# Optimization experiments

Hardware: AMD Instinct MI355X
Metric: run time of the kernel (lower is better)

The kernel has to match this reference:

```python
import jax, jax.numpy as jnp
import numpy as np

D_MODEL = 512
HIDDEN = 2048
N_EXPERTS = 8
TOP_K = 2


def setup_inputs() -> dict:
    key = jax.random.key(0)
    ks = jax.random.split(key, 7)
    B, S = 4, 2048
    s1 = 1.0 / np.sqrt(D_MODEL)
    s2 = 1.0 / np.sqrt(HIDDEN)
    return {
        "x": jax.random.normal(ks[0], (B, S, D_MODEL), dtype=jnp.float32),
        "W1": jax.random.normal(ks[1], (N_EXPERTS, D_MODEL, HIDDEN), dtype=jnp.float32) * s1,
        "b1": jnp.zeros((N_EXPERTS, HIDDEN), dtype=jnp.float32),
        "W2": jax.random.normal(ks[2], (N_EXPERTS, HIDDEN, D_MODEL), dtype=jnp.float32) * s2,
        "b2": jnp.zeros((N_EXPERTS, D_MODEL), dtype=jnp.float32),
        "Wg": jax.random.normal(ks[3], (D_MODEL, N_EXPERTS), dtype=jnp.float32) * s1,
        "bg": jnp.zeros((N_EXPERTS,), dtype=jnp.float32),
    }


def reference(x, W1, b1, W2, b2, Wg, bg):
    # Gate: [B,S,E]
    gate_scores = jnp.einsum("bsd,de->bse", x, Wg) + bg
    topk_scores, topk_idx = jax.lax.top_k(gate_scores, TOP_K)   # [B,S,K]
    topk_weights = jax.nn.softmax(topk_scores, axis=-1)          # [B,S,K]

    # Naive MoE: compute every expert on every token (dropout is identity in eval).
    h = jax.nn.relu(jnp.einsum("bsd,edh->bseh", x, W1) + b1)     # [B,S,E,H]
    expert_outputs = jnp.einsum("bseh,ehd->bsed", h, W2) + b2    # [B,S,E,D]

    # Gather top-k expert outputs and combine.
    topk_out = jnp.take_along_axis(expert_outputs, topk_idx[..., None], axis=-2)  # [B,S,K,D]
    return jnp.sum(topk_out * topk_weights[..., None], axis=-2)  # [B,S,D]
```

## Files before the change

kernel.cpp:

```cpp
#include <hip/hip_runtime.h>
#include <hip/hip_bf16.h>
#include <cstdint>
#include <cstddef>

#define D_MODEL 512
#define HIDDEN  2048
#define N_EXP   8
#define NTOK    8192
#define MAXROWS (NTOK * 2)

typedef unsigned short u16;
typedef _Float16 half8 __attribute__((ext_vector_type(8)));
typedef float   f32x16 __attribute__((ext_vector_type(16)));

__device__ __forceinline__ unsigned pk2(_Float16 a, _Float16 b) {
    unsigned short ua, ub;
    __builtin_memcpy(&ua, &a, 2); __builtin_memcpy(&ub, &b, 2);
    return (unsigned)ua | ((unsigned)ub << 16);
}
__device__ __forceinline__ void split2(float a, float b, unsigned& h, unsigned& l) {
    _Float16 ha = (_Float16)a, hb = (_Float16)b;
    float ra = a - (float)ha, rb = b - (float)hb;
    h = pk2(ha, hb);
    l = pk2((_Float16)ra, (_Float16)rb);
}
__device__ __forceinline__ half8 h8(uint2 lo, uint2 hi) {
    union { unsigned u[4]; half8 h; } t;
    t.u[0] = lo.x; t.u[1] = lo.y; t.u[2] = hi.x; t.u[3] = hi.y;
    return t.h;
}
__device__ __forceinline__ f32x16 mfma16(half8 a, half8 b, f32x16 c) {
    return __builtin_amdgcn_mfma_f32_32x32x16_f16(a, b, c, 0, 0, 0);
}
__device__ __forceinline__ void gload16(const void* g, void* l) {
    __builtin_amdgcn_global_load_lds(
        (const __attribute__((address_space(1))) unsigned int*)g,
        (__attribute__((address_space(3))) unsigned int*)l, 16, 0, 0);
}

__global__ __launch_bounds__(256) void gate_kernel(
    const float* __restrict__ x, const float* __restrict__ Wg,
    const float* __restrict__ bg,
    int* __restrict__ eidx, float* __restrict__ ewt, int* __restrict__ cnt)
{
    const int wid  = threadIdx.x >> 6;
    const int lane = threadIdx.x & 63;
    const int t = blockIdx.x * 4 + wid;
    const float* xr = x + (size_t)t * D_MODEL;

    float p[8] = {0.f,0.f,0.f,0.f,0.f,0.f,0.f,0.f};
    for (int i = lane; i < D_MODEL; i += 64) {
        const float xv = xr[i];
        const float4 a = *(const float4*)(Wg + (size_t)i * 8);
        const float4 b = *(const float4*)(Wg + (size_t)i * 8 + 4);
        p[0] += xv*a.x; p[1] += xv*a.y; p[2] += xv*a.z; p[3] += xv*a.w;
        p[4] += xv*b.x; p[5] += xv*b.y; p[6] += xv*b.z; p[7] += xv*b.w;
    }
    #pragma unroll
    for (int off = 32; off >= 1; off >>= 1) {
        #pragma unroll
        for (int e = 0; e < 8; ++e) p[e] += __shfl_xor(p[e], off, 64);
    }
    if (lane == 0) {
        float s[8];
        #pragma unroll
        for (int e = 0; e < 8; ++e) s[e] = p[e] + bg[e];
        int e1 = 0; float v1 = s[0];
        #pragma unroll
        for (int e = 1; e < 8; ++e) if (s[e] > v1) { v1 = s[e]; e1 = e; }
        int e2 = -1; float v2 = -3.0e38f;
        #pragma unroll
        for (int e = 0; e < 8; ++e) if (e != e1 && s[e] > v2) { v2 = s[e]; e2 = e; }
        const float w1 = 1.f / (1.f + expf(v2 - v1));
        eidx[2*t]   = e1;  eidx[2*t+1] = e2;
        ewt [2*t]   = w1;  ewt [2*t+1] = 1.f - w1;
        atomicAdd(&cnt[e1], 1);
        atomicAdd(&cnt[e2], 1);
    }
}

__global__ void scan_kernel(const int* __restrict__ cnt,
                            int* __restrict__ offs, int* __restrict__ cur)
{
    if (threadIdx.x == 0) {
        int run = 0;
        #pragma unroll
        for (int e = 0; e < 8; ++e) { offs[e] = run; cur[e] = run; run += cnt[e]; }
    }
}

__global__ __launch_bounds__(256) void route_kernel(
    const int* __restrict__ eidx, const float* __restrict__ ewt,
    int* __restrict__ cur, int* __restrict__ rows, float* __restrict__ rwt)
{
    const int t = blockIdx.x * 256 + threadIdx.x;
    if (t >= NTOK) return;
    #pragma unroll
    for (int k = 0; k < 2; ++k) {
        const int e = eidx[2*t + k];
        const int pos = atomicAdd(&cur[e], 1);
        rows[pos] = t;
        rwt [pos] = ewt[2*t + k];
    }
}

__global__ __launch_bounds__(256) void conv_w1(const float* __restrict__ W1,
                                               u16* __restrict__ W1c)
{
    const int e = blockIdx.z;
    const int h0 = blockIdx.x * 64, d0 = blockIdx.y * 64;
    __shared__ float T[64][65];
    const int hl = threadIdx.x & 63, q = threadIdx.x >> 6;
    const float* src = W1 + (size_t)e * D_MODEL * HIDDEN;
    #pragma unroll
    for (int rr = 0; rr < 16; ++rr) {
        const int d = rr*4 + q;
        T[d][hl] = src[(size_t)(d0 + d) * HIDDEN + h0 + hl];
    }
    __syncthreads();
    #pragma unroll
    for (int it = 0; it < 2; ++it) {
        const int dblk = q + 4*it;
        float v[8];
        #pragma unroll
        for (int j = 0; j < 8; ++j) v[j] = T[dblk*8 + j][hl];
        unsigned hh[4], ll[4];
        #pragma unroll
        for (int p = 0; p < 4; ++p) split2(v[2*p], v[2*p+1], hh[p], ll[p]);
        const int gd = d0 + dblk*8, gh = h0 + hl;
        const int hc = gh >> 9, hloc = gh & 511;
        const int ds = gd >> 7, pa = (gd >> 4) & 7, dcb = (gd >> 3) & 1;
        u16* dst = W1c + ((size_t)(((e*4 + hc)*4 + ds)*8 + pa))*16384
                       + dcb*4096 + hloc*8;
        *(uint4*)dst          = make_uint4(hh[0], hh[1], hh[2], hh[3]);
        *(uint4*)(dst + 8192) = make_uint4(ll[0], ll[1], ll[2], ll[3]);
    }
}

__global__ __launch_bounds__(256) void conv_w2(const float* __restrict__ W2,
                                               u16* __restrict__ W2c)
{
    const int e = blockIdx.z;
    const int h0 = blockIdx.x * 64, d0 = blockIdx.y * 64;
    __shared__ float T[64][65];
    const int c63 = threadIdx.x & 63, q = threadIdx.x >> 6;
    const float* src = W2 + (size_t)e * HIDDEN * D_MODEL;
    #pragma unroll
    for (int rr = 0; rr < 16; ++rr) {
        const int h = rr*4 + q;
        T[h][c63] = src[(size_t)(h0 + h) * D_MODEL + d0 + c63];
    }
    __syncthreads();
    #pragma unroll
    for (int it = 0; it < 2; ++it) {
        const int cc = it*256 + threadIdx.x;
        const int hbl = cc >> 5, dp = cc & 31;
        unsigned hh[4], ll[4];
        #pragma unroll
        for (int dd = 0; dd < 2; ++dd) {
            split2(T[hbl*4+0][dp*2+dd], T[hbl*4+1][dp*2+dd], hh[dd*2+0], ll[dd*2+0]);
            split2(T[hbl*4+2][dp*2+dd], T[hbl*4+3][dp*2+dd], hh[dd*2+1], ll[dd*2+1]);
        }
        const int gh = h0 + hbl*4, gd = d0 + dp*2;
        const int hc = gh >> 9, pb = (gh >> 4) & 31, hb = (gh >> 2) & 3;
        u16* dst = W2c + ((size_t)((e*4 + hc)*32 + pb))*16384 + hb*2048 + gd*4;
        *(uint4*)dst          = make_uint4(hh[0], hh[1], hh[2], hh[3]);
        *(uint4*)(dst + 8192) = make_uint4(ll[0], ll[1], ll[2], ll[3]);
    }
}

__global__ __launch_bounds__(512, 2) void moe_mfma(
    const float* __restrict__ x,
    const u16* __restrict__ W1c, const u16* __restrict__ W2c,
    const float* __restrict__ b1, const float* __restrict__ b2,
    const int* __restrict__ cnt, const int* __restrict__ offs,
    const int* __restrict__ rows, const float* __restrict__ rwt,
    float* __restrict__ out)
{
    const int e  = blockIdx.y;
    const int n  = cnt[e];
    const int t0 = blockIdx.x * 64;
    if (t0 >= n) return;
    const int base   = offs[e];
    const int mcount = min(64, n - t0);

    const int tid  = threadIdx.x;
    const int wv   = tid >> 6;
    const int lane = tid & 63;
    const int g    = lane >> 5;
    const int l31  = lane & 31;

    __shared__ __align__(16) u16  Wp[2][16384];
    __shared__ __align__(16) u16  Xs[2][16][64][8];
    __shared__ __align__(16) u16  Hp[2][2][4][64][4];
    __shared__ float b1s[512];
    __shared__ int   toks_s[64];
    __shared__ float wts_s[64];

    if (tid < 64) {
        int tk = 0; float ww = 0.f;
        if (tid < mcount) { tk = rows[base + t0 + tid]; ww = rwt[base + t0 + tid]; }
        toks_s[tid] = tk; wts_s[tid] = ww;
    }
    __syncthreads();

    const float* b1e = b1 + (size_t)e * HIDDEN;

    auto w1p = [&](int hc, int ds, int pa) {
        return W1c + ((size_t)(((e*4 + hc)*4 + ds)*8 + pa)) * 16384;
    };
    auto w2p = [&](int hc, int pb) {
        return W2c + ((size_t)((e*4 + hc)*32 + pb)) * 16384;
    };
    auto stageW = [&](const u16* src, int buf) {
        const char* s = (const char*)src;
        char* d = (char*)&Wp[buf][0];
        #pragma unroll
        for (int k = 0; k < 4; ++k) {
            const int off = (k*8 + wv) * 1024;
            gload16(s + off + lane*16, d + off);
        }
    };
    auto stageX = [&](int ds) {
        const float* xr = x + (size_t)toks_s[lane] * D_MODEL + ds*128 + wv*16;
        const float4 v0 = *(const float4*)(xr + 0), v1 = *(const float4*)(xr + 4);
        const float4 v2 = *(const float4*)(xr + 8), v3 = *(const float4*)(xr + 12);
        unsigned h[4], l[4];
        split2(v0.x, v0.y, h[0], l[0]); split2(v0.z, v0.w, h[1], l[1]);
        split2(v1.x, v1.y, h[2], l[2]); split2(v1.z, v1.w, h[3], l[3]);
        *(uint4*)&Xs[0][wv*2][lane][0]   = make_uint4(h[0], h[1], h[2], h[3]);
        *(uint4*)&Xs[1][wv*2][lane][0]   = make_uint4(l[0], l[1], l[2], l[3]);
        split2(v2.x, v2.y, h[0], l[0]); split2(v2.z, v2.w, h[1], l[1]);
        split2(v3.x, v3.y, h[2], l[2]); split2(v3.z, v3.w, h[3], l[3]);
        *(uint4*)&Xs[0][wv*2+1][lane][0] = make_uint4(h[0], h[1], h[2], h[3]);
        *(uint4*)&Xs[1][wv*2+1][lane][0] = make_uint4(l[0], l[1], l[2], l[3]);
    };

    f32x16 d1[2][2], d2[2][2];
    #pragma unroll
    for (int a = 0; a < 2; ++a)
        #pragma unroll
        for (int b = 0; b < 2; ++b)
            #pragma unroll
            for (int r = 0; r < 16; ++r) d2[a][b][r] = 0.f;

    unsigned hpk[2][2][2][2][4];

    auto writeH = [&](u16* hp, const unsigned (&hk)[2][2][4]) {
        #pragma unroll
        for (int tf = 0; tf < 2; ++tf)
            #pragma unroll
            for (int pl = 0; pl < 2; ++pl) {
                *(uint2*)&hp[((pl*4 + g    )*64 + tf*32 + l31)*4] = make_uint2(hk[tf][pl][0], hk[tf][pl][1]);
                *(uint2*)&hp[((pl*4 + g + 2)*64 + tf*32 + l31)*4] = make_uint2(hk[tf][pl][2], hk[tf][pl][3]);
            }
    };
    auto ownerH = [&](int pn) {
        const int f = pn >> 1;
        if (wv != (f >> 1)) return;
        u16* hp = &Hp[pn & 1][0][0][0][0];
        if (f & 1) { if (pn & 1) writeH(hp, hpk[1][1]); else writeH(hp, hpk[1][0]); }
        else       { if (pn & 1) writeH(hp, hpk[0][1]); else writeH(hp, hpk[0][0]); }
    };

    auto computeA = [&](int cur, int pa) {
        const u16* wp = &Wp[cur][0];
        half8 aw[2][2], bx[2][2];
        #pragma unroll
        for (int mfs = 0; mfs < 2; ++mfs)
            #pragma unroll
            for (int pl = 0; pl < 2; ++pl)
                aw[mfs][pl] = *(const half8*)&wp[pl*8192 + g*4096 + ((2*wv + mfs)*32 + l31)*8];
        #pragma unroll
        for (int tf = 0; tf < 2; ++tf)
            #pragma unroll
            for (int pl = 0; pl < 2; ++pl)
                bx[tf][pl] = *(const half8*)&Xs[pl][2*pa + g][tf*32 + l31][0];
        #pragma unroll
        for (int mfs = 0; mfs < 2; ++mfs)
            #pragma unroll
            for (int tf = 0; tf < 2; ++tf) {
                d1[mfs][tf] = mfma16(aw[mfs][0], bx[tf][0], d1[mfs][tf]);
                d1[mfs][tf] = mfma16(aw[mfs][0], bx[tf][1], d1[mfs][tf]);
                d1[mfs][tf] = mfma16(aw[mfs][1], bx[tf][0], d1[mfs][tf]);
            }
    };
    auto computeB = [&](int cur, int pb) {
        const u16* wp = &Wp[cur][0];
        const u16* hp = &Hp[pb & 1][0][0][0][0];
        half8 aw[2][2], bh[2][2];
        #pragma unroll
        for (int mfs = 0; mfs < 2; ++mfs)
            #pragma unroll
            for (int pl = 0; pl < 2; ++pl) {
                const int d = (2*wv + mfs)*32 + l31;
                uint2 lo = *(const uint2*)&wp[pl*8192 + (g    )*2048 + d*4];
                uint2 hi = *(const uint2*)&wp[pl*8192 + (g + 2)*2048 + d*4];
                aw[mfs][pl] = h8(lo, hi);
            }
        #pragma unroll
        for (int tf = 0; tf < 2; ++tf)
            #pragma unroll
            for (int pl = 0; pl < 2; ++pl) {
                uint2 lo = *(const uint2*)&hp[((pl*4 + g    )*64 + tf*32 + l31)*4];
                uint2 hi = *(const uint2*)&hp[((pl*4 + g + 2)*64 + tf*32 + l31)*4];
                bh[tf][pl] = h8(lo, hi);
            }
        #pragma unroll
        for (int mfs = 0; mfs < 2; ++mfs)
            #pragma unroll
            for (int tf = 0; tf < 2; ++tf) {
                d2[mfs][tf] = mfma16(aw[mfs][0], bh[tf][0], d2[mfs][tf]);
                d2[mfs][tf] = mfma16(aw[mfs][0], bh[tf][1], d2[mfs][tf]);
                d2[mfs][tf] = mfma16(aw[mfs][1], bh[tf][0], d2[mfs][tf]);
            }
    };
    auto finishH = [&]() {
        #pragma unroll
        for (int mfs = 0; mfs < 2; ++mfs) {
            const int hbase = (2*wv + mfs) * 32;
            #pragma unroll
            for (int tf = 0; tf < 2; ++tf) {
                const float wt = wts_s[tf*32 + l31];
                float t[16];
                #pragma unroll
                for (int r = 0; r < 16; ++r) {
                    const int ho = (r & 3) + 8*(r >> 2) + 4*g;
                    t[r] = fmaxf(d1[mfs][tf][r] + b1s[hbase + ho], 0.f) * wt;
                }
                #pragma unroll
                for (int c = 0; c < 2; ++c)
                    #pragma unroll
                    for (int q = 0; q < 4; ++q)
                        split2(t[8*c + 2*q], t[8*c + 2*q + 1],
                               hpk[mfs][c][tf][0][q], hpk[mfs][c][tf][1][q]);
            }
        }
    };

    stageX(0);
    stageW(w1p(0, 0, 0), 0);
    int cur = 0;
    __syncthreads();

    #pragma unroll 1
    for (int hc = 0; hc < 4; ++hc) {
        b1s[tid] = b1e[hc*512 + tid];
        #pragma unroll
        for (int a = 0; a < 2; ++a)
            #pragma unroll
            for (int b = 0; b < 2; ++b)
                #pragma unroll
                for (int r = 0; r < 16; ++r) d1[a][b][r] = 0.f;

        #pragma unroll 1
        for (int ds = 0; ds < 4; ++ds) {
            #pragma unroll 2
            for (int pa = 0; pa < 8; ++pa) {
                if (pa < 7)      stageW(w1p(hc, ds, pa + 1), cur ^ 1);
                else if (ds < 3) stageW(w1p(hc, ds + 1, 0),  cur ^ 1);
                else             stageW(w2p(hc, 0),          cur ^ 1);
                computeA(cur, pa);
                if (pa == 7 && ds < 3) stageX(ds + 1);
                __syncthreads();
                cur ^= 1;
            }
        }

        finishH();
        ownerH(0);
        __syncthreads();

        #pragma unroll 2
        for (int pb = 0; pb < 32; ++pb) {
            if (pb < 31)     stageW(w2p(hc, pb + 1),    cur ^ 1);
            else if (hc < 3) stageW(w1p(hc + 1, 0, 0),  cur ^ 1);
            if (pb < 31) ownerH(pb + 1);
            computeB(cur, pb);
            if (pb == 31 && hc < 3) stageX(0);
            __syncthreads();
            cur ^= 1;
        }
    }

    float* Ot = (float*)&Wp[0][0];
    const float* b2e = b2 + (size_t)e * D_MODEL;
    #pragma unroll 1
    for (int c = 0; c < 4; ++c) {
        if ((wv >> 1) == c) {
            #pragma unroll
            for (int mfs = 0; mfs < 2; ++mfs)
                #pragma unroll
                for (int tf = 0; tf < 2; ++tf)
                    #pragma unroll
                    for (int r = 0; r < 16; ++r) {
                        const int dl = (wv & 1)*64 + mfs*32 + (r & 3) + 8*(r >> 2) + 4*g;
                        Ot[(tf*32 + l31)*129 + dl] = d2[mfs][tf][r];
                    }
        }
        __syncthreads();
        #pragma unroll
        for (int it = 0; it < 16; ++it) {
            const int flat = it*512 + tid;
            const int tk = flat >> 7, dl = flat & 127;
            if (tk < mcount)
                atomicAdd(out + (size_t)toks_s[tk]*D_MODEL + c*128 + dl,
                          Ot[tk*129 + dl] + wts_s[tk]*b2e[c*128 + dl]);
        }
        __syncthreads();
    }
}

__global__ __launch_bounds__(512) void moe_fp32(
    const float* __restrict__ x,
    const float* __restrict__ W1, const float* __restrict__ b1,
    const float* __restrict__ W2, const float* __restrict__ b2,
    const int* __restrict__ cnt, const int* __restrict__ offs,
    const int* __restrict__ rows, const float* __restrict__ rwt,
    float* __restrict__ out)
{
    const int e  = blockIdx.y;
    const int n  = cnt[e];
    const int t0 = blockIdx.x * 32;
    if (t0 >= n) return;
    const int base   = offs[e];
    const int mcount = min(32, n - t0);

    __shared__ float Xs[32 * 512];
    __shared__ float Ws[32 * 512];
    __shared__ float Hs[32 * 36];
    __shared__ int   toks[32];
    __shared__ float wts[32];

    const int tid  = threadIdx.x;
    const int w    = tid >> 6;
    const int lane = tid & 63;

    if (tid < 32) {
        int tk = 0; float ww = 0.f;
        if (tid < mcount) { tk = rows[base + t0 + tid]; ww = rwt[base + t0 + tid]; }
        toks[tid] = tk; wts[tid] = ww;
    }
    __syncthreads();

    float4* Xs4 = (float4*)Xs;
    for (int i = tid; i < 32 * 128; i += 512) {
        const int m = i >> 7, c4 = i & 127;
        float4 v = make_float4(0.f, 0.f, 0.f, 0.f);
        if (m < mcount) v = *(const float4*)(x + (size_t)toks[m] * D_MODEL + c4 * 4);
        Xs4[m * 128 + (c4 ^ (m & 7))] = v;
    }

    const int mA = (lane & 15) | ((w & 1) << 4);
    const int hA = ((w >> 1) << 3) | ((lane >> 4) << 1);
    const int sx = mA & 7;
    const int s0 = (hA >> 2) & 7;
    const int mB = (w & 1) << 4;
    const int dB = ((w >> 1) << 7) + lane * 2;

    float2 acc[16];
    #pragma unroll
    for (int mi = 0; mi < 16; ++mi) acc[mi] = make_float2(0.f, 0.f);

    const float* W1e = W1 + (size_t)e * (D_MODEL * HIDDEN);
    const float* W2e = W2 + (size_t)e * (HIDDEN * D_MODEL);
    const float* b1e = b1 + (size_t)e * HIDDEN;

    const int hq     = tid & 7;
    const int dstage = tid >> 3;
    float4* Ws4 = (float4*)Ws;

    for (int hcc = 0; hcc < HIDDEN / 32; ++hcc) {
        const int h0 = hcc * 32;
        {
            const float* src = W1e + h0 + hq * 4;
            #pragma unroll
            for (int pp = 0; pp < 8; ++pp) {
                const int d = pp * 64 + dstage;
                const float4 v = *(const float4*)(src + (size_t)d * HIDDEN);
                const int dsz = d ^ (hq << 2);
                Ws[(hq * 4 + 0) * 512 + dsz] = v.x;
                Ws[(hq * 4 + 1) * 512 + dsz] = v.y;
                Ws[(hq * 4 + 2) * 512 + dsz] = v.z;
                Ws[(hq * 4 + 3) * 512 + dsz] = v.w;
            }
        }
        __syncthreads();
        {
            const float4* Xr  = Xs4 + mA * 128;
            const float4* Wr0 = Ws4 + hA * 128;
            const float4* Wr1 = Ws4 + (hA + 1) * 128;
            float4 A0 = make_float4(0,0,0,0), A1 = make_float4(0,0,0,0);
            #pragma unroll 4
            for (int d4 = 0; d4 < 128; ++d4) {
                const float4 xv = Xr[d4 ^ sx];
                const float4 u  = Wr0[d4 ^ s0];
                const float4 vv = Wr1[d4 ^ s0];
                A0.x += xv.x*u.x;  A0.y += xv.y*u.y;  A0.z += xv.z*u.z;  A0.w += xv.w*u.w;
                A1.x += xv.x*vv.x; A1.y += xv.y*vv.y; A1.z += xv.z*vv.z; A1.w += xv.w*vv.w;
            }
            const float a0 = (A0.x + A0.y) + (A0.z + A0.w);
            const float a1 = (A1.x + A1.y) + (A1.z + A1.w);
            const float ww = wts[mA];
            Hs[mA * 36 + hA]     = fmaxf(a0 + b1e[h0 + hA],     0.f) * ww;
            Hs[mA * 36 + hA + 1] = fmaxf(a1 + b1e[h0 + hA + 1], 0.f) * ww;
        }
        __syncthreads();
        {
            const float* w2ptr = W2e + (size_t)h0 * D_MODEL + dB;
            #pragma unroll
            for (int qq = 0; qq < 8; ++qq) {
                const float2 wv0 = *(const float2*)(w2ptr + (size_t)(qq*4 + 0) * D_MODEL);
                const float2 wv1 = *(const float2*)(w2ptr + (size_t)(qq*4 + 1) * D_MODEL);
                const float2 wv2 = *(const float2*)(w2ptr + (size_t)(qq*4 + 2) * D_MODEL);
                const float2 wv3 = *(const float2*)(w2ptr + (size_t)(qq*4 + 3) * D_MODEL);
                #pragma unroll
                for (int mi = 0; mi < 16; ++mi) {
                    const float4 hv = *(const float4*)&Hs[(mB + mi) * 36 + qq * 4];
                    acc[mi].x += hv.x*wv0.x + hv.y*wv1.x + hv.z*wv2.x + hv.w*wv3.x;
                    acc[mi].y += hv.x*wv0.y + hv.y*wv1.y + hv.z*wv2.y + hv.w*wv3.y;
                }
            }
        }
    }

    const float2 b2v = *(const float2*)(b2 + (size_t)e * D_MODEL + dB);
    #pragma unroll
    for (int mi = 0; mi < 16; ++mi) {
        const int m = mB + mi;
        if (m < mcount) {
            const float ww = wts[m];
            float* op = out + (size_t)toks[m] * D_MODEL + dB;
            atomicAdd(op,     acc[mi].x + ww * b2v.x);
            atomicAdd(op + 1, acc[mi].y + ww * b2v.y);
        }
    }
}

extern "C" void kernel_launch(void* const* d_in, const int* in_sizes, int n_in,
                              void* d_out, int out_size, void* d_ws, size_t ws_size,
                              hipStream_t stream)
{
    const float* x  = (const float*)d_in[0];
    const float* W1 = (const float*)d_in[1];
    const float* b1 = (const float*)d_in[2];
    const float* W2 = (const float*)d_in[3];
    const float* b2 = (const float*)d_in[4];
    const float* Wg = (const float*)d_in[5];
    const float* bg = (const float*)d_in[6];
    float* out = (float*)d_out;

    const size_t WC_BYTES = (size_t)1024 * 32768;
    const size_t NEED = 2 * WC_BYTES + (1u << 20);
    const bool fast = (ws_size >= NEED);

    char* wsc = (char*)d_ws;
    u16* W1c = (u16*)wsc;
    u16* W2c = (u16*)(wsc + WC_BYTES);
    char* rbase = fast ? (wsc + 2 * WC_BYTES) : wsc;

    int*   cnt  = (int*)rbase;
    int*   offs = cnt + 8;
    int*   curp = offs + 8;
    int*   eidx = curp + 8;
    float* ewt  = (float*)(eidx + 2 * NTOK);
    int*   rows = (int*)(ewt + 2 * NTOK);
    float* rwt  = (float*)(rows + MAXROWS);

    hipMemsetAsync(cnt, 0, 24 * sizeof(int), stream);
    hipMemsetAsync(d_out, 0, (size_t)out_size * sizeof(float), stream);

    gate_kernel <<<NTOK / 4,   256, 0, stream>>>(x, Wg, bg, eidx, ewt, cnt);
    scan_kernel <<<1,          64,  0, stream>>>(cnt, offs, curp);
    route_kernel<<<NTOK / 256, 256, 0, stream>>>(eidx, ewt, curp, rows, rwt);

    if (fast) {
        conv_w1<<<dim3(32, 8, 8), 256, 0, stream>>>(W1, W1c);
        conv_w2<<<dim3(32, 8, 8), 256, 0, stream>>>(W2, W2c);
        moe_mfma<<<dim3(128, 8), 512, 0, stream>>>(x, W1c, W2c, b1, b2,
                                                   cnt, offs, rows, rwt, out);
    } else {
        moe_fp32<<<dim3(512, 8), 512, 0, stream>>>(x, W1, b1, W2, b2,
                                                   cnt, offs, rows, rwt, out);
    }
}
```

Baseline: 897.2 us.

## Split MoE hidden dim across blocks with compact tile table and register-streamed weights

Each block now handles one (expert, token-tile, hidden-chunk) work item listed in a compact tile table built by the scan kernel, so four times as many blocks share the work and padding tiles exit early. Weights are laid out so each wave loads its MFMA A-operands straight from global memory into double-buffered registers, replacing the LDS weight staging and many block barriers. The x staging is split into load and write phases and double-buffered, and MFMA sections run at raised priority. In exchange, every hidden chunk issues its own atomic adds into the output, which raises atomic traffic fourfold, and weight reads bypass LDS sharing.

```diff
diff --git a/kernel.cpp b/kernel.cpp
--- a/kernel.cpp
+++ b/kernel.cpp
@@ -8,10 +8,14 @@
 #define N_EXP   8
 #define NTOK    8192
 #define MAXROWS (NTOK * 2)
+#define MAXT2   1056
 
 typedef unsigned short u16;
 typedef _Float16 half8 __attribute__((ext_vector_type(8)));
 typedef float   f32x16 __attribute__((ext_vector_type(16)));
+
+#define SBAR()  __builtin_amdgcn_s_barrier()
+#define LGKM0() asm volatile("s_waitcnt lgkmcnt(0)" ::: "memory")
 
 __device__ __forceinline__ unsigned pk2(_Float16 a, _Float16 b) {
     unsigned short ua, ub;
@@ -29,13 +33,11 @@
     t.u[0] = lo.x; t.u[1] = lo.y; t.u[2] = hi.x; t.u[3] = hi.y;
     return t.h;
 }
+__device__ __forceinline__ half8 h8c(uint4 v) {
+    union { uint4 u; half8 h; } t; t.u = v; return t.h;
+}
 __device__ __forceinline__ f32x16 mfma16(half8 a, half8 b, f32x16 c) {
     return __builtin_amdgcn_mfma_f32_32x32x16_f16(a, b, c, 0, 0, 0);
-}
-__device__ __forceinline__ void gload16(const void* g, void* l) {
-    __builtin_amdgcn_global_load_lds(
-        (const __attribute__((address_space(1))) unsigned int*)g,
-        (__attribute__((address_space(3))) unsigned int*)l, 16, 0, 0);
 }
 
 __global__ __launch_bounds__(256) void gate_kernel(
@@ -79,13 +81,36 @@
     }
 }
 
-__global__ void scan_kernel(const int* __restrict__ cnt,
-                            int* __restrict__ offs, int* __restrict__ cur)
-{
-    if (threadIdx.x == 0) {
+__global__ __launch_bounds__(1024) void scan_kernel(
+    const int* __restrict__ cnt, int* __restrict__ offs, int* __restrict__ cur,
+    int* __restrict__ tileTab)
+{
+    __shared__ int nt[8];
+    const int t = threadIdx.x;
+    if (t == 0) {
         int run = 0;
         #pragma unroll
-        for (int e = 0; e < 8; ++e) { offs[e] = run; cur[e] = run; run += cnt[e]; }
+        for (int e = 0; e < 8; ++e) {
+            offs[e] = run; cur[e] = run; run += cnt[e];
+            nt[e] = (cnt[e] + 63) >> 6;
+        }
+    }
+    __syncthreads();
+    {
+        const int e = t & 7, i = t >> 3;
+        const int hcv = i >> 5, sv = i & 31;
+        tileTab[t] = (sv < nt[e]) ? ((e << 24) | (sv << 8) | hcv) : -1;
+    }
+    if (t < MAXT2 - 1024) tileTab[1024 + t] = -1;
+    __syncthreads();
+    if (t == 0) {
+        int fp = 0;
+        for (int e = 0; e < 8; ++e)
+            for (int sv = 32; sv < nt[e]; ++sv)
+                for (int hcv = 0; hcv < 4; ++hcv) {
+                    while (tileTab[fp] >= 0) ++fp;
+                    tileTab[fp] = (e << 24) | (sv << 8) | hcv;
+                }
     }
 }
 
@@ -108,30 +133,29 @@
                                                u16* __restrict__ W1c)
 {
     const int e = blockIdx.z;
-    const int h0 = blockIdx.x * 64, d0 = blockIdx.y * 64;
+    const int gh0 = blockIdx.x * 64;
+    const int d0  = blockIdx.y * 64;
     __shared__ float T[64][65];
-    const int hl = threadIdx.x & 63, q = threadIdx.x >> 6;
+    const int hl = threadIdx.x & 63, q4 = threadIdx.x >> 6;
     const float* src = W1 + (size_t)e * D_MODEL * HIDDEN;
     #pragma unroll
     for (int rr = 0; rr < 16; ++rr) {
-        const int d = rr*4 + q;
-        T[d][hl] = src[(size_t)(d0 + d) * HIDDEN + h0 + hl];
-    }
-    __syncthreads();
-    #pragma unroll
-    for (int it = 0; it < 2; ++it) {
-        const int dblk = q + 4*it;
+        const int d = rr*4 + q4;
+        T[d][hl] = src[(size_t)(d0 + d) * HIDDEN + gh0 + hl];
+    }
+    __syncthreads();
+    const int hc = gh0 >> 9, hloc0 = gh0 & 511;
+    const int q0 = d0 >> 4;
+    #pragma unroll
+    for (int g = 0; g < 2; ++g) {
         float v[8];
         #pragma unroll
-        for (int j = 0; j < 8; ++j) v[j] = T[dblk*8 + j][hl];
+        for (int j = 0; j < 8; ++j) v[j] = T[q4*16 + g*8 + j][hl];
         unsigned hh[4], ll[4];
         #pragma unroll
         for (int p = 0; p < 4; ++p) split2(v[2*p], v[2*p+1], hh[p], ll[p]);
-        const int gd = d0 + dblk*8, gh = h0 + hl;
-        const int hc = gh >> 9, hloc = gh & 511;
-        const int ds = gd >> 7, pa = (gd >> 4) & 7, dcb = (gd >> 3) & 1;
-        u16* dst = W1c + ((size_t)(((e*4 + hc)*4 + ds)*8 + pa))*16384
-                       + dcb*4096 + hloc*8;
+        u16* dst = W1c + ((((size_t)(e*4 + hc)*32 + (q0 + q4))*2 + 0)*2 + g)*4096
+                       + (size_t)(hloc0 + hl)*8;
         *(uint4*)dst          = make_uint4(hh[0], hh[1], hh[2], hh[3]);
         *(uint4*)(dst + 8192) = make_uint4(ll[0], ll[1], ll[2], ll[3]);
     }
@@ -141,29 +165,31 @@
                                                u16* __restrict__ W2c)
 {
     const int e = blockIdx.z;
-    const int h0 = blockIdx.x * 64, d0 = blockIdx.y * 64;
+    const int gh0 = blockIdx.x * 64;
+    const int d0  = blockIdx.y * 64;
     __shared__ float T[64][65];
-    const int c63 = threadIdx.x & 63, q = threadIdx.x >> 6;
+    const int dl = threadIdx.x & 63, s4 = threadIdx.x >> 6;
     const float* src = W2 + (size_t)e * HIDDEN * D_MODEL;
     #pragma unroll
     for (int rr = 0; rr < 16; ++rr) {
-        const int h = rr*4 + q;
-        T[h][c63] = src[(size_t)(h0 + h) * D_MODEL + d0 + c63];
-    }
-    __syncthreads();
-    #pragma unroll
-    for (int it = 0; it < 2; ++it) {
-        const int cc = it*256 + threadIdx.x;
-        const int hbl = cc >> 5, dp = cc & 31;
+        const int h = rr*4 + s4;
+        T[h][dl] = src[(size_t)(gh0 + h) * D_MODEL + d0 + dl];
+    }
+    __syncthreads();
+    const int hc = gh0 >> 9, r0 = (gh0 & 511) >> 4;
+    #pragma unroll
+    for (int g = 0; g < 2; ++g) {
+        float v[8];
+        #pragma unroll
+        for (int j = 0; j < 8; ++j) {
+            const int h_loc = (g + 2*(j >> 2))*4 + (j & 3);
+            v[j] = T[s4*16 + h_loc][dl];
+        }
         unsigned hh[4], ll[4];
         #pragma unroll
-        for (int dd = 0; dd < 2; ++dd) {
-            split2(T[hbl*4+0][dp*2+dd], T[hbl*4+1][dp*2+dd], hh[dd*2+0], ll[dd*2+0]);
-            split2(T[hbl*4+2][dp*2+dd], T[hbl*4+3][dp*2+dd], hh[dd*2+1], ll[dd*2+1]);
-        }
-        const int gh = h0 + hbl*4, gd = d0 + dp*2;
-        const int hc = gh >> 9, pb = (gh >> 4) & 31, hb = (gh >> 2) & 3;
-        u16* dst = W2c + ((size_t)((e*4 + hc)*32 + pb))*16384 + hb*2048 + gd*4;
+        for (int p = 0; p < 4; ++p) split2(v[2*p], v[2*p+1], hh[p], ll[p]);
+        u16* dst = W2c + ((((size_t)(e*4 + hc)*32 + (r0 + s4))*2 + 0)*2 + g)*4096
+                       + (size_t)(d0 + dl)*8;
         *(uint4*)dst          = make_uint4(hh[0], hh[1], hh[2], hh[3]);
         *(uint4*)(dst + 8192) = make_uint4(ll[0], ll[1], ll[2], ll[3]);
     }
@@ -175,13 +201,17 @@
     const float* __restrict__ b1, const float* __restrict__ b2,
     const int* __restrict__ cnt, const int* __restrict__ offs,
     const int* __restrict__ rows, const float* __restrict__ rwt,
+    const int* __restrict__ tileTab,
     float* __restrict__ out)
 {
-    const int e  = blockIdx.y;
+    const int tv = tileTab[blockIdx.x];
+    if (tv < 0) return;
+    const int e  = tv >> 24;
+    const int s  = (tv >> 8) & 0xff;
+    const int hc = tv & 3;
     const int n  = cnt[e];
-    const int t0 = blockIdx.x * 64;
-    if (t0 >= n) return;
-    const int base   = offs[e];
+    const int base = offs[e];
+    const int t0 = s << 6;
     const int mcount = min(64, n - t0);
 
     const int tid  = threadIdx.x;
@@ -190,10 +220,8 @@
     const int g    = lane >> 5;
     const int l31  = lane & 31;
 
-    __shared__ __align__(16) u16  Wp[2][16384];
-    __shared__ __align__(16) u16  Xs[2][16][64][8];
+    __shared__ __align__(16) u16  Xs[2][2][16][64][8];
     __shared__ __align__(16) u16  Hp[2][2][4][64][4];
-    __shared__ float b1s[512];
     __shared__ int   toks_s[64];
     __shared__ float wts_s[64];
 
@@ -204,36 +232,36 @@
     }
     __syncthreads();
 
-    const float* b1e = b1 + (size_t)e * HIDDEN;
-
-    auto w1p = [&](int hc, int ds, int pa) {
-        return W1c + ((size_t)(((e*4 + hc)*4 + ds)*8 + pa)) * 16384;
-    };
-    auto w2p = [&](int hc, int pb) {
-        return W2c + ((size_t)((e*4 + hc)*32 + pb)) * 16384;
-    };
-    auto stageW = [&](const u16* src, int buf) {
-        const char* s = (const char*)src;
-        char* d = (char*)&Wp[buf][0];
-        #pragma unroll
-        for (int k = 0; k < 4; ++k) {
-            const int off = (k*8 + wv) * 1024;
-            gload16(s + off + lane*16, d + off);
-        }
-    };
-    auto stageX = [&](int ds) {
-        const float* xr = x + (size_t)toks_s[lane] * D_MODEL + ds*128 + wv*16;
-        const float4 v0 = *(const float4*)(xr + 0), v1 = *(const float4*)(xr + 4);
-        const float4 v2 = *(const float4*)(xr + 8), v3 = *(const float4*)(xr + 12);
+    const u16* W1b = W1c + (size_t)(e*4 + hc) * 32 * 16384;
+    const u16* W2b = W2c + (size_t)(e*4 + hc) * 32 * 16384;
+    const int rA0 = (2*wv + 0)*32 + l31;
+    const int rA1 = (2*wv + 1)*32 + l31;
+
+    auto ldW = [&](const u16* Wb, uint4 (&aw)[2][2], int q) {
+        const u16* p = Wb + (size_t)q * 16384 + g * 4096;
+        aw[0][0] = *(const uint4*)(p +        (size_t)rA0 * 8);
+        aw[0][1] = *(const uint4*)(p + 8192 + (size_t)rA0 * 8);
+        aw[1][0] = *(const uint4*)(p +        (size_t)rA1 * 8);
+        aw[1][1] = *(const uint4*)(p + 8192 + (size_t)rA1 * 8);
+    };
+
+    float4 xr0, xr1, xr2, xr3;
+    auto stageX_load = [&](int ds) {
+        const float* xp = x + (size_t)toks_s[lane] * D_MODEL + ds*128 + wv*16;
+        xr0 = *(const float4*)(xp + 0);  xr1 = *(const float4*)(xp + 4);
+        xr2 = *(const float4*)(xp + 8);  xr3 = *(const float4*)(xp + 12);
+    };
+    auto stageX_write = [&](int ds) {
+        const int sb = ds & 1;
         unsigned h[4], l[4];
-        split2(v0.x, v0.y, h[0], l[0]); split2(v0.z, v0.w, h[1], l[1]);
-        split2(v1.x, v1.y, h[2], l[2]); split2(v1.z, v1.w, h[3], l[3]);
-        *(uint4*)&Xs[0][wv*2][lane][0]   = make_uint4(h[0], h[1], h[2], h[3]);
-        *(uint4*)&Xs[1][wv*2][lane][0]   = make_uint4(l[0], l[1], l[2], l[3]);
-        split2(v2.x, v2.y, h[0], l[0]); split2(v2.z, v2.w, h[1], l[1]);
-        split2(v3.x, v3.y, h[2], l[2]); split2(v3.z, v3.w, h[3], l[3]);
-        *(uint4*)&Xs[0][wv*2+1][lane][0] = make_uint4(h[0], h[1], h[2], h[3]);
-        *(uint4*)&Xs[1][wv*2+1][lane][0] = make_uint4(l[0], l[1], l[2], l[3]);
+        split2(xr0.x, xr0.y, h[0], l[0]); split2(xr0.z, xr0.w, h[1], l[1]);
+        split2(xr1.x, xr1.y, h[2], l[2]); split2(xr1.z, xr1.w, h[3], l[3]);
+        *(uint4*)&Xs[sb][0][wv*2][lane][0]   = make_uint4(h[0], h[1], h[2], h[3]);
+        *(uint4*)&Xs[sb][1][wv*2][lane][0]   = make_uint4(l[0], l[1], l[2], l[3]);
+        split2(xr2.x, xr2.y, h[0], l[0]); split2(xr2.z, xr2.w, h[1], l[1]);
+        split2(xr3.x, xr3.y, h[2], l[2]); split2(xr3.z, xr3.w, h[3], l[3]);
+        *(uint4*)&Xs[sb][0][wv*2+1][lane][0] = make_uint4(h[0], h[1], h[2], h[3]);
+        *(uint4*)&Xs[sb][1][wv*2+1][lane][0] = make_uint4(l[0], l[1], l[2], l[3]);
     };
 
     f32x16 d1[2][2], d2[2][2];
@@ -242,7 +270,7 @@
         #pragma unroll
         for (int b = 0; b < 2; ++b)
             #pragma unroll
-            for (int r = 0; r < 16; ++r) d2[a][b][r] = 0.f;
+            for (int r = 0; r < 16; ++r) { d1[a][b][r] = 0.f; d2[a][b][r] = 0.f; }
 
     unsigned hpk[2][2][2][2][4];
 
@@ -256,48 +284,36 @@
             }
     };
     auto ownerH = [&](int pn) {
-        const int f = pn >> 1;
-        if (wv != (f >> 1)) return;
+        if (wv != (pn >> 2)) return;
         u16* hp = &Hp[pn & 1][0][0][0][0];
-        if (f & 1) { if (pn & 1) writeH(hp, hpk[1][1]); else writeH(hp, hpk[1][0]); }
-        else       { if (pn & 1) writeH(hp, hpk[0][1]); else writeH(hp, hpk[0][0]); }
-    };
-
-    auto computeA = [&](int cur, int pa) {
-        const u16* wp = &Wp[cur][0];
-        half8 aw[2][2], bx[2][2];
-        #pragma unroll
-        for (int mfs = 0; mfs < 2; ++mfs)
+        const int mfs = (pn >> 1) & 1;
+        if (mfs) { if (pn & 1) writeH(hp, hpk[1][1]); else writeH(hp, hpk[1][0]); }
+        else     { if (pn & 1) writeH(hp, hpk[0][1]); else writeH(hp, hpk[0][0]); }
+    };
+
+    auto computeA = [&](const uint4 (&A)[2][2], int sb, int pa) {
+        half8 bx[2][2];
+        #pragma unroll
+        for (int tf = 0; tf < 2; ++tf)
             #pragma unroll
             for (int pl = 0; pl < 2; ++pl)
-                aw[mfs][pl] = *(const half8*)&wp[pl*8192 + g*4096 + ((2*wv + mfs)*32 + l31)*8];
-        #pragma unroll
-        for (int tf = 0; tf < 2; ++tf)
-            #pragma unroll
-            for (int pl = 0; pl < 2; ++pl)
-                bx[tf][pl] = *(const half8*)&Xs[pl][2*pa + g][tf*32 + l31][0];
-        #pragma unroll
-        for (int mfs = 0; mfs < 2; ++mfs)
+                bx[tf][pl] = *(const half8*)&Xs[sb][pl][2*pa + g][tf*32 + l31][0];
+        __builtin_amdgcn_s_setprio(1);
+        #pragma unroll
+        for (int mfs = 0; mfs < 2; ++mfs) {
+            const half8 a0 = h8c(A[mfs][0]), a1 = h8c(A[mfs][1]);
             #pragma unroll
             for (int tf = 0; tf < 2; ++tf) {
-                d1[mfs][tf] = mfma16(aw[mfs][0], bx[tf][0], d1[mfs][tf]);
-                d1[mfs][tf] = mfma16(aw[mfs][0], bx[tf][1], d1[mfs][tf]);
-                d1[mfs][tf] = mfma16(aw[mfs][1], bx[tf][0], d1[mfs][tf]);
-            }
-    };
-    auto computeB = [&](int cur, int pb) {
-        const u16* wp = &Wp[cur][0];
-        const u16* hp = &Hp[pb & 1][0][0][0][0];
-        half8 aw[2][2], bh[2][2];
-        #pragma unroll
-        for (int mfs = 0; mfs < 2; ++mfs)
-            #pragma unroll
-            for (int pl = 0; pl < 2; ++pl) {
-                const int d = (2*wv + mfs)*32 + l31;
-                uint2 lo = *(const uint2*)&wp[pl*8192 + (g    )*2048 + d*4];
-                uint2 hi = *(const uint2*)&wp[pl*8192 + (g + 2)*2048 + d*4];
-                aw[mfs][pl] = h8(lo, hi);
-            }
+                d1[mfs][tf] = mfma16(a0, bx[tf][0], d1[mfs][tf]);
+                d1[mfs][tf] = mfma16(a0, bx[tf][1], d1[mfs][tf]);
+                d1[mfs][tf] = mfma16(a1, bx[tf][0], d1[mfs][tf]);
+            }
+        }
+        __builtin_amdgcn_s_setprio(0);
+    };
+    auto computeB = [&](const uint4 (&A)[2][2], int rb) {
+        const u16* hp = &Hp[rb][0][0][0][0];
+        half8 bh[2][2];
         #pragma unroll
         for (int tf = 0; tf < 2; ++tf)
             #pragma unroll
@@ -306,28 +322,35 @@
                 uint2 hi = *(const uint2*)&hp[((pl*4 + g + 2)*64 + tf*32 + l31)*4];
                 bh[tf][pl] = h8(lo, hi);
             }
-        #pragma unroll
-        for (int mfs = 0; mfs < 2; ++mfs)
+        __builtin_amdgcn_s_setprio(1);
+        #pragma unroll
+        for (int mfs = 0; mfs < 2; ++mfs) {
+            const half8 a0 = h8c(A[mfs][0]), a1 = h8c(A[mfs][1]);
             #pragma unroll
             for (int tf = 0; tf < 2; ++tf) {
-                d2[mfs][tf] = mfma16(aw[mfs][0], bh[tf][0], d2[mfs][tf]);
-                d2[mfs][tf] = mfma16(aw[mfs][0], bh[tf][1], d2[mfs][tf]);
-                d2[mfs][tf] = mfma16(aw[mfs][1], bh[tf][0], d2[mfs][tf]);
-            }
+                d2[mfs][tf] = mfma16(a0, bh[tf][0], d2[mfs][tf]);
+                d2[mfs][tf] = mfma16(a0, bh[tf][1], d2[mfs][tf]);
+                d2[mfs][tf] = mfma16(a1, bh[tf][0], d2[mfs][tf]);
+            }
+        }
+        __builtin_amdgcn_s_setprio(0);
     };
     auto finishH = [&]() {
+        const float* b1p = b1 + (size_t)e * HIDDEN + hc * 512;
         #pragma unroll
         for (int mfs = 0; mfs < 2; ++mfs) {
             const int hbase = (2*wv + mfs) * 32;
+            float bias[16];
+            #pragma unroll
+            for (int r = 0; r < 16; ++r)
+                bias[r] = b1p[hbase + (r & 3) + 8*(r >> 2) + 4*g];
             #pragma unroll
             for (int tf = 0; tf < 2; ++tf) {
                 const float wt = wts_s[tf*32 + l31];
                 float t[16];
                 #pragma unroll
-                for (int r = 0; r < 16; ++r) {
-                    const int ho = (r & 3) + 8*(r >> 2) + 4*g;
-                    t[r] = fmaxf(d1[mfs][tf][r] + b1s[hbase + ho], 0.f) * wt;
-                }
+                for (int r = 0; r < 16; ++r)
+                    t[r] = fmaxf(d1[mfs][tf][r] + bias[r], 0.f) * wt;
                 #pragma unroll
                 for (int c = 0; c < 2; ++c)
                     #pragma unroll
@@ -338,52 +361,35 @@
         }
     };
 
-    stageX(0);
-    stageW(w1p(0, 0, 0), 0);
-    int cur = 0;
-    __syncthreads();
-
-    #pragma unroll 1
-    for (int hc = 0; hc < 4; ++hc) {
-        b1s[tid] = b1e[hc*512 + tid];
-        #pragma unroll
-        for (int a = 0; a < 2; ++a)
-            #pragma unroll
-            for (int b = 0; b < 2; ++b)
-                #pragma unroll
-                for (int r = 0; r < 16; ++r) d1[a][b][r] = 0.f;
-
-        #pragma unroll 1
-        for (int ds = 0; ds < 4; ++ds) {
-            #pragma unroll 2
-            for (int pa = 0; pa < 8; ++pa) {
-                if (pa < 7)      stageW(w1p(hc, ds, pa + 1), cur ^ 1);
-                else if (ds < 3) stageW(w1p(hc, ds + 1, 0),  cur ^ 1);
-                else             stageW(w2p(hc, 0),          cur ^ 1);
-                computeA(cur, pa);
-                if (pa == 7 && ds < 3) stageX(ds + 1);
-                __syncthreads();
-                cur ^= 1;
-            }
-        }
-
-        finishH();
-        ownerH(0);
-        __syncthreads();
-
-        #pragma unroll 2
-        for (int pb = 0; pb < 32; ++pb) {
-            if (pb < 31)     stageW(w2p(hc, pb + 1),    cur ^ 1);
-            else if (hc < 3) stageW(w1p(hc + 1, 0, 0),  cur ^ 1);
-            if (pb < 31) ownerH(pb + 1);
-            computeB(cur, pb);
-            if (pb == 31 && hc < 3) stageX(0);
-            __syncthreads();
-            cur ^= 1;
-        }
-    }
-
-    float* Ot = (float*)&Wp[0][0];
+    uint4 awp[2][2][2];
+    ldW(W1b, awp[0], 0);
+    stageX_load(0);
+    stageX_write(0);
+    __syncthreads();
+
+    #pragma unroll 2
+    for (int q = 0; q < 32; ++q) {
+        const int pa = q & 7, ds = q >> 3;
+        if (q < 31) ldW(W1b, awp[(q + 1) & 1], q + 1);
+        else        ldW(W2b, awp[(q + 1) & 1], 0);
+        computeA(awp[q & 1], ds & 1, pa);
+        if (pa == 4 && ds < 3) stageX_load(ds + 1);
+        if (pa == 5 && ds < 3) stageX_write(ds + 1);
+        if (pa == 7 && ds < 3) { LGKM0(); SBAR(); }
+    }
+
+    finishH();
+    ownerH(0);
+    LGKM0(); SBAR();
+
+    #pragma unroll 2
+    for (int r = 0; r < 32; ++r) {
+        if (r < 31) { ldW(W2b, awp[(r + 1) & 1], r + 1); ownerH(r + 1); }
+        computeB(awp[r & 1], r & 1);
+        LGKM0(); SBAR();
+    }
+
+    float* Ot = (float*)&Xs[0][0][0][0][0];
     const float* b2e = b2 + (size_t)e * D_MODEL;
     #pragma unroll 1
     for (int c = 0; c < 4; ++c) {
@@ -403,9 +409,11 @@
         for (int it = 0; it < 16; ++it) {
             const int flat = it*512 + tid;
             const int tk = flat >> 7, dl = flat & 127;
-            if (tk < mcount)
-                atomicAdd(out + (size_t)toks_s[tk]*D_MODEL + c*128 + dl,
-                          Ot[tk*129 + dl] + wts_s[tk]*b2e[c*128 + dl]);
+            if (tk < mcount) {
+                float v = Ot[tk*129 + dl];
+                if (hc == 0) v += wts_s[tk] * b2e[c*128 + dl];
+                atomicAdd(out + (size_t)toks_s[tk]*D_MODEL + c*128 + dl, v);
+            }
         }
         __syncthreads();
     }
@@ -566,19 +574,20 @@
     float* ewt  = (float*)(eidx + 2 * NTOK);
     int*   rows = (int*)(ewt + 2 * NTOK);
     float* rwt  = (float*)(rows + MAXROWS);
+    int*   tileTab = (int*)(rwt + MAXROWS);
 
     hipMemsetAsync(cnt, 0, 24 * sizeof(int), stream);
     hipMemsetAsync(d_out, 0, (size_t)out_size * sizeof(float), stream);
 
-    gate_kernel <<<NTOK / 4,   256, 0, stream>>>(x, Wg, bg, eidx, ewt, cnt);
-    scan_kernel <<<1,          64,  0, stream>>>(cnt, offs, curp);
-    route_kernel<<<NTOK / 256, 256, 0, stream>>>(eidx, ewt, curp, rows, rwt);
+    gate_kernel <<<NTOK / 4,   256,  0, stream>>>(x, Wg, bg, eidx, ewt, cnt);
+    scan_kernel <<<1,          1024, 0, stream>>>(cnt, offs, curp, tileTab);
+    route_kernel<<<NTOK / 256, 256,  0, stream>>>(eidx, ewt, curp, rows, rwt);
 
     if (fast) {
         conv_w1<<<dim3(32, 8, 8), 256, 0, stream>>>(W1, W1c);
         conv_w2<<<dim3(32, 8, 8), 256, 0, stream>>>(W2, W2c);
-        moe_mfma<<<dim3(128, 8), 512, 0, stream>>>(x, W1c, W2c, b1, b2,
-                                                   cnt, offs, rows, rwt, out);
+        moe_mfma<<<MAXT2, 512, 0, stream>>>(x, W1c, W2c, b1, b2,
+                                            cnt, offs, rows, rwt, tileTab, out);
     } else {
         moe_fp32<<<dim3(512, 8), 512, 0, stream>>>(x, W1, b1, W2, b2,
                                                    cnt, offs, rows, rwt, out);
```

Result: slower. 1.310 ms (+46.0%).
